# Kernel tuning notes

Measured on AMD Instinct MI355X. Metric: run time of the kernel, lower is better.

The kernel has to match this reference:

```python
import jax, jax.numpy as jnp
import numpy as np

T, K, V, B = 12, 50, 5000, 256
RHO, HT, HE = 300, 800, 256
DELTA, LAM = 0.005, 0.01
CLIP_LO, CLIP_HI = -100.0, 100.0


def setup_inputs():
    key = jax.random.key(0)
    ks = jax.random.split(key, 16)
    s = 0.02  # weight init scale
    rn = lambda k, sh, sc=s: jax.random.normal(k, sh) * sc
    return dict(
        normalized_bows=jax.random.uniform(ks[0], (B, V)),
        bow_t=jax.random.uniform(ks[1], (B, T, V)),
        adj_mat=jax.random.uniform(ks[2], (V, V)) * 0.01,
        mu_q_alpha=rn(ks[3], (K, T, RHO), 0.1),
        logsigma_q_alpha=rn(ks[4], (K, T, RHO), 0.1),
        rho_W=rn(ks[5], (V, RHO)), rho_b=jnp.zeros((V,)),
        qt_W1=rn(ks[6], (HT, V + K)), qt_b1=jnp.zeros((HT,)),
        qt_W2=rn(ks[7], (HT, HT)), qt_b2=jnp.zeros((HT,)),
        mut_W=rn(ks[8], (K, HT)), mut_b=jnp.zeros((K,)),
        lst_W=rn(ks[9], (K, HT)), lst_b=jnp.zeros((K,)),
        qe_W=rn(ks[10], (HE, V)), qe_b=jnp.zeros((HE,)),
        Wih=rn(ks[11], (4 * HE, HE)), Whh=rn(ks[12], (4 * HE, HE)),
        bih=jnp.zeros((4 * HE,)), bhh=jnp.zeros((4 * HE,)),
        mue_W=rn(ks[13], (K, HE + K)), mue_b=jnp.zeros((K,)),
        lse_W=rn(ks[14], (K, HE + K)), lse_b=jnp.zeros((K,)),
    )


def _kl(q_mu, q_ls, p_mu, p_ls):
    # KL(N(q_mu, e^{q_ls}) || N(p_mu, e^{p_ls})), logsigma == log-variance as in the torch code
    q_ls = jnp.clip(q_ls, CLIP_LO, CLIP_HI)
    kl = (jnp.exp(q_ls) + (q_mu - p_mu) ** 2) / (jnp.exp(p_ls) + 1e-6) - 1.0 + p_ls - q_ls
    return 0.5 * kl.sum(-1).mean()


def _forward(normalized_bows, bow_t, adj_mat, mu_q_alpha, logsigma_q_alpha,
             rho_W, rho_b, qt_W1, qt_b1, qt_W2, qt_b2, mut_W, mut_b,
             lst_W, lst_b, qe_W, qe_b, Wih, Whh, bih, bhh,
             mue_W, mue_b, lse_W, lse_b):
    ek = jax.random.split(jax.random.key(42), 3)

    # ---- get_alpha: samples are t-independent, KL chains through previous sample ----
    mu_a = jnp.transpose(mu_q_alpha, (1, 0, 2))        # [T,K,R]
    ls_a = jnp.transpose(logsigma_q_alpha, (1, 0, 2))  # [T,K,R]
    eps_a = jax.random.normal(ek[0], (T, K, RHO))
    alphas = mu_a + eps_a * jnp.exp(0.5 * ls_a)        # [T,K,R]
    p_mu_a = jnp.concatenate([jnp.zeros((1, K, RHO)), alphas[:-1]], 0)
    p_ls_a = jnp.concatenate([jnp.zeros((1, 1, 1)),
                              jnp.full((T - 1, 1, 1), jnp.log(DELTA))], 0)
    q_ls = jnp.clip(ls_a, CLIP_LO, CLIP_HI)
    kl_a = (jnp.exp(q_ls) + (mu_a - p_mu_a) ** 2) / (jnp.exp(p_ls_a) + 1e-6) - 1.0 + p_ls_a - q_ls
    kld_alpha = (0.5 * kl_a.sum(-1).mean(-1)).mean()   # per-t mean over K, then mean over T

    # ---- get_beta: rho Linear + softmax over vocab -> [T,K,V] ----
    beta = jax.nn.softmax(jnp.einsum('tkr,vr->tkv', alphas, rho_W) + rho_b, axis=-1)

    # ---- get_eta: LSTM over time + sequential reparameterized recurrence ----
    inp = jnp.einsum('btv,hv->bth', bow_t, qe_W) + qe_b  # [B,T,HE]

    def lstm_step(carry, x_t):
        h, c = carry
        g = x_t @ Wih.T + bih + h @ Whh.T + bhh          # [B,4HE]
        i, f, gg, o = jnp.split(g, 4, axis=-1)           # PyTorch gate order i,f,g,o
        c = jax.nn.sigmoid(f) * c + jax.nn.sigmoid(i) * jnp.tanh(gg)
        h = jax.nn.sigmoid(o) * jnp.tanh(c)
        return (h, c), h

    h0 = (jnp.zeros((B, HE)), jnp.zeros((B, HE)))
    _, lstm_out = jax.lax.scan(lstm_step, h0, jnp.transpose(inp, (1, 0, 2)))  # [T,B,HE]

    eps_e = jax.random.normal(ek[1], (T, B, K))
    # prior log-variance: 0 at t=0 (N(0,I)), log(delta) afterwards
    p_ls_e = jnp.concatenate([jnp.zeros((1,)), jnp.full((T - 1,), jnp.log(DELTA))])

    def eta_step(eta_prev, xs):
        o_t, eps_t, pls_t = xs
        z = jnp.concatenate([o_t, eta_prev], -1)         # [B,HE+K]
        mu = z @ mue_W.T + mue_b
        ls = z @ lse_W.T + lse_b
        eta_t = mu + eps_t * jnp.exp(0.5 * ls)
        kl_t = _kl(mu, ls, eta_prev, pls_t)              # eta_prev==0 at t=0, matching torch
        return eta_t, (eta_t, kl_t)

    _, (etas, kl_e) = jax.lax.scan(eta_step, jnp.zeros((B, K)), (lstm_out, eps_e, p_ls_e))
    kld_eta = kl_e.sum()                                  # etas: [T,B,K]

    # ---- get_theta: MLP encoder (enc_drop=0 -> dropout branch skipped) ----
    bows = jnp.broadcast_to(normalized_bows, (T, B, V))
    x = jnp.concatenate([bows, etas], -1)                 # [T,B,V+K]
    h = jax.nn.relu(x @ qt_W1.T + qt_b1)
    h = jax.nn.relu(h @ qt_W2.T + qt_b2)
    mu_t = h @ mut_W.T + mut_b
    ls_t = h @ lst_W.T + lst_b
    z = mu_t + jax.random.normal(ek[2], (T, B, K)) * jnp.exp(0.5 * ls_t)
    theta = jax.nn.softmax(z, axis=-1)                    # [T,B,K]
    kld_theta = _kl(mu_t, ls_t, etas, jnp.zeros((K,)))

    # ---- decode / nll ----
    bow_tT = jnp.transpose(bow_t, (1, 0, 2))              # [T,B,V]
    lik = jnp.einsum('tbk,tkv->tbv', theta, beta)
    nll = (10.0 * (-(jnp.log(lik + 1e-6)) * bow_tT).sum(-1).mean(-1)).sum()

    # ---- adjacency constraint: -lambda * trace(beta_t @ A @ beta_t^T) summed over t ----
    tmp = jnp.einsum('tkv,vw->tkw', beta, adj_mat)
    cond_loss = (-(LAM * (tmp * beta).sum((1, 2)))).sum()

    return nll, kld_theta, kld_alpha, kld_eta, cond_loss


def reference(normalized_bows, bow_t, adj_mat, mu_q_alpha, logsigma_q_alpha,
              rho_W, rho_b, qt_W1, qt_b1, qt_W2, qt_b2, mut_W, mut_b,
              lst_W, lst_b, qe_W, qe_b, Wih, Whh, bih, bhh,
              mue_W, mue_b, lse_W, lse_b):
    return _forward(normalized_bows, bow_t, adj_mat, mu_q_alpha, logsigma_q_alpha,
                    rho_W, rho_b, qt_W1, qt_b1, qt_W2, qt_b2, mut_W, mut_b,
                    lst_W, lst_b, qe_W, qe_b, Wih, Whh, bih, bhh,
                    mue_W, mue_b, lse_W, lse_b)
```

## Files before the change

### kernel.cpp

```cpp
#include <hip/hip_runtime.h>
#include <stdint.h>

#define TT 12
#define KK 50
#define VV 5000
#define BB 256
#define RHO_ 300
#define HT_ 800
#define HE_ 256
#define LOG_DELTA -5.2983174f
#define DENOM0 (1.0f + 1e-6f)
#define DENOM1 (0.005f + 1e-6f)

typedef __attribute__((ext_vector_type(8))) short short8;
typedef __attribute__((ext_vector_type(4))) float f32x4;

__host__ __device__ inline void threefry2x32(uint32_t k0, uint32_t k1,
                                             uint32_t x0, uint32_t x1,
                                             uint32_t& o0, uint32_t& o1) {
  uint32_t ks2 = k0 ^ k1 ^ 0x1BD11BDAu;
  x0 += k0; x1 += k1;
#define TF_RND(r) { x0 += x1; x1 = (x1 << r) | (x1 >> (32 - r)); x1 ^= x0; }
  TF_RND(13) TF_RND(15) TF_RND(26) TF_RND(6)  x0 += k1;  x1 += ks2 + 1u;
  TF_RND(17) TF_RND(29) TF_RND(16) TF_RND(24) x0 += ks2; x1 += k0 + 2u;
  TF_RND(13) TF_RND(15) TF_RND(26) TF_RND(6)  x0 += k0;  x1 += k1 + 3u;
  TF_RND(17) TF_RND(29) TF_RND(16) TF_RND(24) x0 += k1;  x1 += ks2 + 4u;
  TF_RND(13) TF_RND(15) TF_RND(26) TF_RND(6)  x0 += ks2; x1 += k0 + 5u;
#undef TF_RND
  o0 = x0; o1 = x1;
}

__device__ inline float erfinv_f(float x) {
  float w = -log1pf(-x * x);
  float p;
  if (w < 5.0f) {
    w -= 2.5f;
    p = 2.81022636e-08f;
    p = fmaf(p, w, 3.43273939e-07f);
    p = fmaf(p, w, -3.5233877e-06f);
    p = fmaf(p, w, -4.39150654e-06f);
    p = fmaf(p, w, 0.00021858087f);
    p = fmaf(p, w, -0.00125372503f);
    p = fmaf(p, w, -0.00417768164f);
    p = fmaf(p, w, 0.246640727f);
    p = fmaf(p, w, 1.50140941f);
  } else {
    w = sqrtf(w) - 3.0f;
    p = -0.000200214257f;
    p = fmaf(p, w, 0.000100950558f);
    p = fmaf(p, w, 0.00134934322f);
    p = fmaf(p, w, -0.00367342844f);
    p = fmaf(p, w, 0.00573950773f);
    p = fmaf(p, w, -0.0076224613f);
    p = fmaf(p, w, 0.00943887047f);
    p = fmaf(p, w, 1.00167406f);
    p = fmaf(p, w, 2.83297682f);
  }
  return p * x;
}

__device__ inline float jax_normal_f(uint32_t k0, uint32_t k1, uint32_t idx) {
  uint32_t o0, o1, bits;
  threefry2x32(k0, k1, 0u, idx, o0, o1);
  bits = o0 ^ o1;
  float f = __uint_as_float((bits >> 9) | 0x3f800000u) - 1.0f;
  const float lo = -0.99999994f;
  float u = fmaf(f, 2.0f, lo);
  u = fmaxf(lo, u);
  return 1.41421356f * erfinv_f(u);
}

__device__ inline float sigmoidf_(float x) { return 1.0f / (1.0f + expf(-x)); }

__device__ inline short f2bf(float f) {
  uint32_t x = __float_as_uint(f);
  uint32_t r = (x + 0x7fffu + ((x >> 16) & 1u)) >> 16;
  return (short)r;
}
__device__ inline float bf2f(short u) {
  return __uint_as_float(((uint32_t)(uint16_t)u) << 16);
}

__device__ inline void blockReduceAtomicAdd(float v, double* target, float* redbuf) {
  int lane = threadIdx.x & 63, wid = threadIdx.x >> 6;
  #pragma unroll
  for (int off = 32; off; off >>= 1) v += __shfl_down(v, off, 64);
  if (lane == 0) redbuf[wid] = v;
  __syncthreads();
  if (threadIdx.x == 0) {
    float tot = redbuf[0] + redbuf[1] + redbuf[2] + redbuf[3];
    atomicAdd(target, (double)tot);
  }
}

template<int MODE, int AF32>
__global__ __launch_bounds__(256) void mfma_gemm(
    const void* __restrict__ Ap, const short* __restrict__ Bp,
    float* __restrict__ C, const float* __restrict__ bias,
    const short* __restrict__ aux, double* __restrict__ slot,
    int M, int N, int K, int lda, int ldb, int ldc, int ldaux,
    int kchunk, int relu)
{
  __shared__ alignas(16) short As[128 * 40];
  __shared__ alignas(16) short Bs[128 * 40];
  __shared__ float redg[4];
  int tid = threadIdx.x, lane = tid & 63, wv = tid >> 6;
  int wm = wv >> 1, wn = wv & 1;
  int quad = lane >> 4, l16 = lane & 15;
  int m0 = blockIdx.y * 128, n0 = blockIdx.x * 128;
  int kbeg = (kchunk > 0) ? (int)blockIdx.z * kchunk : 0;
  int kend = (kchunk > 0) ? min(K, kbeg + kchunk) : K;
  const short* Ab = (const short*)Ap;
  const float* Af = (const float*)Ap;

  f32x4 acc[16];
  #pragma unroll
  for (int i = 0; i < 16; i++) acc[i] = (f32x4){0.f, 0.f, 0.f, 0.f};

  int srow = tid >> 2, skc = (tid & 3) * 8;
  for (int k0 = kbeg; k0 < kend; k0 += 32) {
    #pragma unroll
    for (int p = 0; p < 2; p++) {
      int row = srow + p * 64;
      int gk = k0 + skc;
      int rem = kend - gk;
      short8 av = {0, 0, 0, 0, 0, 0, 0, 0};
      int gm = m0 + row;
      if (gm < M && rem > 0) {
        if (AF32) {
          const float* s = Af + (size_t)gm * lda + gk;
          if (rem >= 8) {
            float4 f0 = *(const float4*)(s);
            float4 f1 = *(const float4*)(s + 4);
            av[0] = f2bf(f0.x); av[1] = f2bf(f0.y); av[2] = f2bf(f0.z); av[3] = f2bf(f0.w);
            av[4] = f2bf(f1.x); av[5] = f2bf(f1.y); av[6] = f2bf(f1.z); av[7] = f2bf(f1.w);
          } else {
            for (int e = 0; e < 8; e++) if (e < rem) av[e] = f2bf(s[e]);
          }
        } else {
          const short* s = Ab + (size_t)gm * lda + gk;
          if (rem >= 8) {
            const uint32_t* u = (const uint32_t*)s;
            uint32_t u0 = u[0], u1 = u[1], u2 = u[2], u3 = u[3];
            av[0] = (short)u0; av[1] = (short)(u0 >> 16);
            av[2] = (short)u1; av[3] = (short)(u1 >> 16);
            av[4] = (short)u2; av[5] = (short)(u2 >> 16);
            av[6] = (short)u3; av[7] = (short)(u3 >> 16);
          } else {
            for (int e = 0; e < 8; e++) if (e < rem) av[e] = s[e];
          }
        }
      }
      *(short8*)(&As[row * 40 + skc]) = av;
      short8 bv = {0, 0, 0, 0, 0, 0, 0, 0};
      int gn = n0 + row;
      if (gn < N && rem > 0) {
        const short* s = Bp + (size_t)gn * ldb + gk;
        if (rem >= 8) {
          const uint32_t* u = (const uint32_t*)s;
          uint32_t u0 = u[0], u1 = u[1], u2 = u[2], u3 = u[3];
          bv[0] = (short)u0; bv[1] = (short)(u0 >> 16);
          bv[2] = (short)u1; bv[3] = (short)(u1 >> 16);
          bv[4] = (short)u2; bv[5] = (short)(u2 >> 16);
          bv[6] = (short)u3; bv[7] = (short)(u3 >> 16);
        } else {
          for (int e = 0; e < 8; e++) if (e < rem) bv[e] = s[e];
        }
      }
      *(short8*)(&Bs[row * 40 + skc]) = bv;
    }
    __syncthreads();
    short8 af[4], bfr[4];
    const short* ap = &As[(wm * 64 + l16) * 40 + quad * 8];
    const short* bp = &Bs[(wn * 64 + l16) * 40 + quad * 8];
    #pragma unroll
    for (int i = 0; i < 4; i++) af[i] = *(const short8*)(ap + i * 16 * 40);
    #pragma unroll
    for (int j = 0; j < 4; j++) bfr[j] = *(const short8*)(bp + j * 16 * 40);
    #pragma unroll
    for (int i = 0; i < 4; i++)
      #pragma unroll
      for (int j = 0; j < 4; j++)
        acc[i * 4 + j] = __builtin_amdgcn_mfma_f32_16x16x32_bf16(af[i], bfr[j], acc[i * 4 + j], 0, 0, 0);
    __syncthreads();
  }

  float s = 0.f;
  #pragma unroll
  for (int i = 0; i < 4; i++) {
    int gmb = m0 + wm * 64 + i * 16 + quad * 4;
    #pragma unroll
    for (int j = 0; j < 4; j++) {
      int gn = n0 + wn * 64 + j * 16 + l16;
      f32x4 v = acc[i * 4 + j];
      if (gn >= N) continue;
      if (MODE == 0) {
        float bs = bias ? bias[gn] : 0.f;
        #pragma unroll
        for (int r = 0; r < 4; r++) {
          int gm = gmb + r;
          if (gm < M) {
            float c = v[r] + bs;
            if (relu) c = fmaxf(c, 0.f);
            C[(size_t)gm * ldc + gn] = c;
          }
        }
      } else if (MODE == 1) {
        #pragma unroll
        for (int r = 0; r < 4; r++) {
          int gm = gmb + r;
          if (gm < M) atomicAdd(&C[(size_t)gm * ldc + gn], v[r]);
        }
      } else {
        #pragma unroll
        for (int r = 0; r < 4; r++) {
          int gm = gmb + r;
          if (gm < M) s += v[r] * bf2f(aux[(size_t)gm * ldaux + gn]);
        }
      }
    }
  }
  if (MODE == 2) {
    #pragma unroll
    for (int off = 32; off; off >>= 1) s += __shfl_down(s, off, 64);
    if (lane == 0) redg[wv] = s;
    __syncthreads();
    if (tid == 0) atomicAdd(slot, (double)(redg[0] + redg[1] + redg[2] + redg[3]));
  }
}

__global__ __launch_bounds__(256) void k_decode64(
    const short* __restrict__ theta_bf, const short* __restrict__ betaT,
    const float* __restrict__ bow_t, double* __restrict__ slot) {
  __shared__ alignas(16) short As[64 * 40];
  __shared__ alignas(16) short Bs[64 * 40];
  __shared__ float redg[4];
  int tid = threadIdx.x, lane = tid & 63, wv = tid >> 6;
  int wm = wv >> 1, wn = wv & 1;
  int quad = lane >> 4, l16 = lane & 15;
  int n0 = blockIdx.x * 64, m0 = blockIdx.y * 64, z = blockIdx.z;
  const short* A = theta_bf + (size_t)z * 256 * 56;

  f32x4 acc[2][2];
  #pragma unroll
  for (int i = 0; i < 2; i++)
    #pragma unroll
    for (int j = 0; j < 2; j++) acc[i][j] = (f32x4){0.f, 0.f, 0.f, 0.f};

  int srow = tid >> 2, skc = (tid & 3) * 8;
  #pragma unroll
  for (int k0 = 0; k0 < 64; k0 += 32) {
    int gk = k0 + skc, rem = KK - gk;
    short8 av = {0, 0, 0, 0, 0, 0, 0, 0};
    int gm = m0 + srow;
    if (rem > 0) {
      const short* s = A + (size_t)gm * 56 + gk;
      if (rem >= 8) {
        const uint32_t* u = (const uint32_t*)s;
        uint32_t u0 = u[0], u1 = u[1], u2 = u[2], u3 = u[3];
        av[0] = (short)u0; av[1] = (short)(u0 >> 16);
        av[2] = (short)u1; av[3] = (short)(u1 >> 16);
        av[4] = (short)u2; av[5] = (short)(u2 >> 16);
        av[6] = (short)u3; av[7] = (short)(u3 >> 16);
      } else {
        for (int e = 0; e < 8; e++) if (e < rem) av[e] = s[e];
      }
    }
    *(short8*)(&As[srow * 40 + skc]) = av;
    short8 bv = {0, 0, 0, 0, 0, 0, 0, 0};
    int gn = n0 + srow;
    if (gn < VV && rem > 0) {
      const short* s = betaT + (size_t)gn * 600 + z * KK + gk;
      if (rem >= 8) {
        const uint32_t* u = (const uint32_t*)s;
        uint32_t u0 = u[0], u1 = u[1], u2 = u[2], u3 = u[3];
        bv[0] = (short)u0; bv[1] = (short)(u0 >> 16);
        bv[2] = (short)u1; bv[3] = (short)(u1 >> 16);
        bv[4] = (short)u2; bv[5] = (short)(u2 >> 16);
        bv[6] = (short)u3; bv[7] = (short)(u3 >> 16);
      } else {
        for (int e = 0; e < 8; e++) if (e < rem) bv[e] = s[e];
      }
    }
    *(short8*)(&Bs[srow * 40 + skc]) = bv;
    __syncthreads();
    short8 af[2], bfr[2];
    #pragma unroll
    for (int i = 0; i < 2; i++) af[i] = *(const short8*)(&As[(wm * 32 + i * 16 + l16) * 40 + quad * 8]);
    #pragma unroll
    for (int j = 0; j < 2; j++) bfr[j] = *(const short8*)(&Bs[(wn * 32 + j * 16 + l16) * 40 + quad * 8]);
    #pragma unroll
    for (int i = 0; i < 2; i++)
      #pragma unroll
      for (int j = 0; j < 2; j++)
        acc[i][j] = __builtin_amdgcn_mfma_f32_16x16x32_bf16(af[i], bfr[j], acc[i][j], 0, 0, 0);
    __syncthreads();
  }

  float s = 0.f;
  #pragma unroll
  for (int i = 0; i < 2; i++) {
    int gmb = m0 + wm * 32 + i * 16 + quad * 4;
    #pragma unroll
    for (int j = 0; j < 2; j++) {
      int gn = n0 + wn * 32 + j * 16 + l16;
      if (gn >= VV) continue;
      f32x4 v = acc[i][j];
      #pragma unroll
      for (int r = 0; r < 4; r++) {
        int gm = gmb + r;
        s -= __logf(v[r] + 1e-6f) * bow_t[((size_t)gm * TT + z) * VV + gn];
      }
    }
  }
  #pragma unroll
  for (int off = 32; off; off >>= 1) s += __shfl_down(s, off, 64);
  if (lane == 0) redg[wv] = s;
  __syncthreads();
  if (tid == 0) atomicAdd(slot, (double)(redg[0] + redg[1] + redg[2] + redg[3]));
}

__global__ void k_prep(const float* __restrict__ qe_W, const float* __restrict__ Wih,
                       const float* __restrict__ qt_W2, const float* __restrict__ qt_W1,
                       const float* __restrict__ rho_W, const float* __restrict__ Whh,
                       const float* __restrict__ bih, const float* __restrict__ bhh,
                       const float* __restrict__ qe_b, const float* __restrict__ qt_b1,
                       const float* __restrict__ mut_W, const float* __restrict__ mut_b,
                       const float* __restrict__ lst_W, const float* __restrict__ lst_b,
                       short* __restrict__ qeW_bf, short* __restrict__ Wih_bf,
                       short* __restrict__ qtW2_bf, short* __restrict__ qtW1_bf,
                       short* __restrict__ tail_bf, short* __restrict__ rhoW_bf,
                       float* __restrict__ whhT, float* __restrict__ sumbias,
                       float* __restrict__ inp, float* __restrict__ bows_part,
                       short* __restrict__ headW_bf, float* __restrict__ head_b) {
  const int N0 = 1280000, N1 = 262144, N2 = 640000, N3 = 4000000, N4 = 40000,
            N5 = 1500000, N6 = 262144, N7 = 1024, N8 = 786432, N9 = 204800,
            N10 = 80000, N11 = 100;
  const int total = N0 + N1 + N2 + N3 + N4 + N5 + N6 + N7 + N8 + N9 + N10 + N11;
  for (int i = blockIdx.x * 256 + threadIdx.x; i < total; i += gridDim.x * 256) {
    int idx = i;
    if (idx < N0) { qeW_bf[idx] = f2bf(qe_W[idx]); continue; }
    idx -= N0;
    if (idx < N1) { Wih_bf[idx] = f2bf(Wih[idx]); continue; }
    idx -= N1;
    if (idx < N2) { qtW2_bf[idx] = f2bf(qt_W2[idx]); continue; }
    idx -= N2;
    if (idx < N3) { int r = idx / VV, c = idx % VV;
      qtW1_bf[idx] = f2bf(qt_W1[(size_t)r * (VV + KK) + c]); continue; }
    idx -= N3;
    if (idx < N4) { int r = idx / KK, c = idx % KK;
      tail_bf[idx] = f2bf(qt_W1[(size_t)r * (VV + KK) + VV + c]); continue; }
    idx -= N4;
    if (idx < N5) { rhoW_bf[idx] = f2bf(rho_W[idx]); continue; }
    idx -= N5;
    if (idx < N6) { int h = idx >> 10, j = idx & 1023;
      whhT[idx] = Whh[(size_t)j * HE_ + h]; continue; }
    idx -= N6;
    if (idx < N7) { sumbias[idx] = bih[idx] + bhh[idx]; continue; }
    idx -= N7;
    if (idx < N8) { inp[idx] = qe_b[idx & 255]; continue; }
    idx -= N8;
    if (idx < N9) { bows_part[idx] = qt_b1[idx % 800]; continue; }
    idx -= N9;
    if (idx < N10) { int r = idx / HT_, c = idx % HT_;
      headW_bf[idx] = f2bf(r < KK ? mut_W[(size_t)r * HT_ + c]
                                  : lst_W[(size_t)(r - KK) * HT_ + c]); continue; }
    idx -= N10;
    head_b[idx] = (idx < KK) ? mut_b[idx] : lst_b[idx - KK];
  }
}

__global__ void k_alphas(const float* __restrict__ mu_q, const float* __restrict__ ls_q,
                         short* __restrict__ alph_bf, double* __restrict__ acc,
                         uint32_t ka, uint32_t kb) {
  __shared__ float red[4];
  int i = blockIdx.x * 256 + threadIdx.x;
  float kl = 0.f;
  if (i < TT * KK * RHO_) {
    int t = i / (KK * RHO_);
    int k = (i / RHO_) % KK;
    int r = i % RHO_;
    int src = k * (TT * RHO_) + t * RHO_ + r;
    float mu = mu_q[src], ls = ls_q[src];
    float eps = jax_normal_f(ka, kb, (uint32_t)i);
    float a = mu + eps * expf(0.5f * ls);
    alph_bf[i] = f2bf(a);
    float qls = fminf(fmaxf(ls, -100.f), 100.f);
    float pmu = 0.f, pls = 0.f, denom = DENOM0;
    if (t > 0) {
      int srcp = k * (TT * RHO_) + (t - 1) * RHO_ + r;
      float mup = mu_q[srcp], lsp = ls_q[srcp];
      float epsp = jax_normal_f(ka, kb, (uint32_t)(i - KK * RHO_));
      pmu = mup + epsp * expf(0.5f * lsp);
      pls = LOG_DELTA; denom = DENOM1;
    }
    float d = mu - pmu;
    kl = (expf(qls) + d * d) / denom - 1.0f + pls - qls;
  }
  blockReduceAtomicAdd(kl, &acc[2], red);
}

__global__ void k_softmax_bf(const float* __restrict__ in, short* __restrict__ out, int ncols) {
  int row = blockIdx.x;
  const float* d = in + (size_t)row * ncols;
  short* o = out + (size_t)row * ncols;
  int tid = threadIdx.x;
  __shared__ float red[256];
  float m = -INFINITY;
  for (int v = tid; v < ncols; v += 256) m = fmaxf(m, d[v]);
  red[tid] = m; __syncthreads();
  for (int s = 128; s; s >>= 1) { if (tid < s) red[tid] = fmaxf(red[tid], red[tid + s]); __syncthreads(); }
  float mx = red[0]; __syncthreads();
  float sum = 0.f;
  for (int v = tid; v < ncols; v += 256) sum += __expf(d[v] - mx);
  red[tid] = sum; __syncthreads();
  for (int s = 128; s; s >>= 1) { if (tid < s) red[tid] += red[tid + s]; __syncthreads(); }
  float inv = 1.0f / red[0];
  for (int v = tid; v < ncols; v += 256) o[v] = f2bf(__expf(d[v] - mx) * inv);
}

__global__ __launch_bounds__(256) void k_transpose_bf(const short* __restrict__ in,
                                                      short* __restrict__ out, int R, int Cc) {
  __shared__ short tile[32][33];
  int c0 = blockIdx.x * 32, r0 = blockIdx.y * 32;
  int tx = threadIdx.x & 31, ty = threadIdx.x >> 5;
  for (int rr = ty; rr < 32; rr += 8) {
    int r = r0 + rr, c = c0 + tx;
    tile[rr][tx] = (r < R && c < Cc) ? in[(size_t)r * Cc + c] : (short)0;
  }
  __syncthreads();
  for (int cc = ty; cc < 32; cc += 8) {
    int c = c0 + cc, r = r0 + tx;
    if (c < Cc && r < R) out[(size_t)c * R + r] = tile[tx][cc];
  }
}

__global__ __launch_bounds__(1024) void k_lstm_all(
    const float* __restrict__ xg, const float* __restrict__ whhT,
    float* __restrict__ lstm_out) {
  __shared__ float hprev[4][256];
  __shared__ float g_s[4][1024];
  int tid = threadIdx.x;
  int b0 = blockIdx.x * 4;
  float c[4] = {0.f, 0.f, 0.f, 0.f};
  if (tid < 256) {
    #pragma unroll
    for (int bb = 0; bb < 4; bb++) hprev[bb][tid] = 0.f;
  }
  __syncthreads();
  for (int t = 0; t < TT; t++) {
    float a0 = 0.f, a1 = 0.f, a2 = 0.f, a3 = 0.f;
    #pragma unroll 8
    for (int h = 0; h < 256; h++) {
      float w = whhT[(size_t)h * 1024 + tid];
      a0 = fmaf(w, hprev[0][h], a0);
      a1 = fmaf(w, hprev[1][h], a1);
      a2 = fmaf(w, hprev[2][h], a2);
      a3 = fmaf(w, hprev[3][h], a3);
    }
    __syncthreads();
    g_s[0][tid] = xg[((size_t)(b0 + 0) * TT + t) * 1024 + tid] + a0;
    g_s[1][tid] = xg[((size_t)(b0 + 1) * TT + t) * 1024 + tid] + a1;
    g_s[2][tid] = xg[((size_t)(b0 + 2) * TT + t) * 1024 + tid] + a2;
    g_s[3][tid] = xg[((size_t)(b0 + 3) * TT + t) * 1024 + tid] + a3;
    __syncthreads();
    if (tid < 256) {
      #pragma unroll
      for (int bb = 0; bb < 4; bb++) {
        float gi = g_s[bb][tid], gf = g_s[bb][256 + tid];
        float gc = g_s[bb][512 + tid], go = g_s[bb][768 + tid];
        c[bb] = sigmoidf_(gf) * c[bb] + sigmoidf_(gi) * tanhf(gc);
        float h = sigmoidf_(go) * tanhf(c[bb]);
        hprev[bb][tid] = h;
        lstm_out[((size_t)t * BB + b0 + bb) * 256 + tid] = h;
      }
    }
    __syncthreads();
  }
}

__global__ __launch_bounds__(128) void k_eta_all(
    const float* __restrict__ lstm_out, const float* __restrict__ mue_W,
    const float* __restrict__ mue_b, const float* __restrict__ lse_W,
    const float* __restrict__ lse_b, float* __restrict__ etas,
    double* __restrict__ acc, uint32_t ka, uint32_t kb) {
  __shared__ float wmu[KK * 306];
  __shared__ float wls[KK * 306];
  __shared__ float z[HE_ + KK];
  __shared__ float mu_s[KK], ls_s[KK];
  int b = blockIdx.x, tid = threadIdx.x;
  for (int i = tid; i < KK * 306; i += 128) { wmu[i] = mue_W[i]; wls[i] = lse_W[i]; }
  float klsum = 0.f;
  if (tid < KK) z[HE_ + tid] = 0.f;
  __syncthreads();
  for (int t = 0; t < TT; t++) {
    for (int i = tid; i < HE_; i += 128) z[i] = lstm_out[((size_t)t * BB + b) * HE_ + i];
    __syncthreads();
    if (tid < 100) {
      int j = tid % KK; bool isMu = tid < KK;
      const float* w = (isMu ? wmu : wls) + j * 306;
      float a = 0.f, a2 = 0.f;
      for (int i = 0; i < HE_ + KK; i += 2) {
        a = fmaf(z[i], w[i], a);
        a2 = fmaf(z[i + 1], w[i + 1], a2);
      }
      a += a2 + (isMu ? mue_b : lse_b)[j];
      if (isMu) mu_s[j] = a; else ls_s[j] = a;
    }
    __syncthreads();
    if (tid < KK) {
      float mu = mu_s[tid], ls = ls_s[tid];
      float eps = jax_normal_f(ka, kb, (uint32_t)((t * BB + b) * KK + tid));
      float eta = mu + eps * expf(0.5f * ls);
      float qls = fminf(fmaxf(ls, -100.f), 100.f);
      float pmu = z[HE_ + tid];
      float pls = (t == 0) ? 0.f : LOG_DELTA;
      float denom = (t == 0) ? DENOM0 : DENOM1;
      float d = mu - pmu;
      klsum += (expf(qls) + d * d) / denom - 1.0f + pls - qls;
      etas[((size_t)t * BB + b) * KK + tid] = eta;
      z[HE_ + tid] = eta;
    }
    __syncthreads();
  }
  if (tid < 64) {
    #pragma unroll
    for (int off = 32; off; off >>= 1) klsum += __shfl_down(klsum, off, 64);
    if (tid == 0) atomicAdd(&acc[3], (double)klsum);
  }
}

__global__ __launch_bounds__(256) void k_h1(
    const float* __restrict__ etas, const short* __restrict__ tail_bf,
    const float* __restrict__ bows_part, short* __restrict__ h1_bf) {
  __shared__ float el[8][KK];
  int m0 = blockIdx.x * 8, tid = threadIdx.x;
  for (int idx = tid; idx < 8 * KK; idx += 256) {
    int mm = idx / KK, kk = idx % KK;
    el[mm][kk] = etas[(size_t)(m0 + mm) * KK + kk];
  }
  __syncthreads();
  for (int j = tid; j < HT_; j += 256) {
    const uint32_t* w = (const uint32_t*)(tail_bf + (size_t)j * KK);
    float wv[KK];
    #pragma unroll
    for (int k = 0; k < KK / 2; k++) {
      uint32_t u = w[k];
      wv[2 * k] = bf2f((short)u); wv[2 * k + 1] = bf2f((short)(u >> 16));
    }
    #pragma unroll
    for (int mm = 0; mm < 8; mm++) {
      int m = m0 + mm, b = m & (BB - 1);
      float a = bows_part[(size_t)b * HT_ + j];
      #pragma unroll
      for (int k = 0; k < KK; k++) a = fmaf(el[mm][k], wv[k], a);
      h1_bf[(size_t)m * HT_ + j] = f2bf(fmaxf(a, 0.f));
    }
  }
}

__global__ __launch_bounds__(64) void k_theta2(
    const float* __restrict__ mu_ls, const float* __restrict__ etas,
    short* __restrict__ theta_bf, double* __restrict__ acc, uint32_t ka, uint32_t kb) {
  int m = blockIdx.x, tid = threadIdx.x;
  float kl = 0.f, zv = -INFINITY;
  if (tid < KK) {
    float mu = mu_ls[(size_t)m * 100 + tid];
    float ls = mu_ls[(size_t)m * 100 + KK + tid];
    float eps = jax_normal_f(ka, kb, (uint32_t)(m * KK + tid));
    zv = mu + eps * expf(0.5f * ls);
    float qls = fminf(fmaxf(ls, -100.f), 100.f);
    float e = etas[(size_t)m * KK + tid];
    float d = mu - e;
    kl = (expf(qls) + d * d) / DENOM0 - 1.0f - qls;
  }
  float mx = zv;
  #pragma unroll
  for (int off = 32; off; off >>= 1) mx = fmaxf(mx, __shfl_xor(mx, off, 64));
  float ev = (tid < KK) ? expf(zv - mx) : 0.f;
  float sum = ev;
  #pragma unroll
  for (int off = 32; off; off >>= 1) sum += __shfl_xor(sum, off, 64);
  if (tid < KK) theta_bf[(size_t)m * 56 + tid] = f2bf(ev / sum);
  #pragma unroll
  for (int off = 32; off; off >>= 1) kl += __shfl_down(kl, off, 64);
  if (tid == 0) atomicAdd(&acc[1], (double)kl);
}

__global__ void k_final(const double* __restrict__ acc, float* __restrict__ out) {
  if (threadIdx.x == 0 && blockIdx.x == 0) {
    out[0] = (float)(acc[0] * (10.0 / (double)BB));
    out[1] = (float)(acc[1] * (0.5 / ((double)TT * (double)BB)));
    out[2] = (float)(acc[2] * (0.5 / ((double)TT * (double)KK)));
    out[3] = (float)(acc[3] * (0.5 / (double)BB));
    out[4] = (float)(acc[4] * (-0.01));
  }
}

extern "C" void kernel_launch(void* const* d_in, const int* in_sizes, int n_in,
                              void* d_out, int out_size, void* d_ws, size_t ws_size,
                              hipStream_t stream) {
  const float* normalized_bows = (const float*)d_in[0];
  const float* bow_t  = (const float*)d_in[1];
  const float* adj    = (const float*)d_in[2];
  const float* mu_q   = (const float*)d_in[3];
  const float* ls_q   = (const float*)d_in[4];
  const float* rho_W  = (const float*)d_in[5];
  const float* rho_b  = (const float*)d_in[6];
  const float* qt_W1  = (const float*)d_in[7];
  const float* qt_b1  = (const float*)d_in[8];
  const float* qt_W2  = (const float*)d_in[9];
  const float* qt_b2  = (const float*)d_in[10];
  const float* mut_W  = (const float*)d_in[11];
  const float* mut_b  = (const float*)d_in[12];
  const float* lst_W  = (const float*)d_in[13];
  const float* lst_b  = (const float*)d_in[14];
  const float* qe_W   = (const float*)d_in[15];
  const float* qe_b   = (const float*)d_in[16];
  const float* Wih    = (const float*)d_in[17];
  const float* Whh    = (const float*)d_in[18];
  const float* bih    = (const float*)d_in[19];
  const float* bhh    = (const float*)d_in[20];
  const float* mue_W  = (const float*)d_in[21];
  const float* mue_b  = (const float*)d_in[22];
  const float* lse_W  = (const float*)d_in[23];
  const float* lse_b  = (const float*)d_in[24];
  float* out = (float*)d_out;

  double* acc = (double*)d_ws;
  float* p          = (float*)d_ws + 16;
  float* betaT_f    = p;               p += 1500000;
  float* beta_bf_f  = p;               p += 1500000;
  float* alphbf_f   = p;               p += 90000;
  float* rhoWbf_f   = p;               p += 750000;
  float* arenaA     = p;               p += 3145728;
  float* qeWbf_f    = p;               p += 640000;
  float* Wihbf_f    = p;               p += 131072;
  float* arenaB     = p;               p += 2320000;
  float* tailbf_f   = p;               p += 20000;
  float* poolC      = p;               p += 2621440;
  float* sumbias    = p;               p += 1024;
  float* etas       = p;               p += 153600;
  float* bows_part  = p;               p += 204800;
  float* thbf_f     = p;               p += 86016;
  float* headWbf_f  = p;               p += 40000;
  float* head_b     = p;               p += 104;
  float* mu_ls      = p;               p += 307200;

  short* betaT    = (short*)betaT_f;
  short* beta_bf  = (short*)beta_bf_f;
  short* alph_bf  = (short*)alphbf_f;
  short* rhoW_bf  = (short*)rhoWbf_f;
  float* logits   = arenaA;
  float* xg       = arenaA;
  short* qeW_bf   = (short*)qeWbf_f;
  short* Wih_bf   = (short*)Wihbf_f;
  short* qtW1_bf  = (short*)arenaB;
  short* qtW2_bf  = (short*)(arenaB + 2000000);
  short* h1_bf    = (short*)arenaB;
  short* tail_bf  = (short*)tailbf_f;
  float* inp      = poolC;
  float* whhT     = poolC + 786432;
  float* lstm_out = poolC + 786432 + 1048576;
  float* h2       = poolC;
  short* theta_bf = (short*)thbf_f;
  short* headW_bf = (short*)headWbf_f;

  uint32_t e0a, e0b, e1a, e1b, e2a, e2b;
  threefry2x32(0u, 42u, 0u, 0u, e0a, e0b);
  threefry2x32(0u, 42u, 0u, 1u, e1a, e1b);
  threefry2x32(0u, 42u, 0u, 2u, e2a, e2b);

  (void)hipMemsetAsync(acc, 0, 5 * sizeof(double), stream);

  k_prep<<<8192, 256, 0, stream>>>(qe_W, Wih, qt_W2, qt_W1, rho_W, Whh, bih, bhh,
                                   qe_b, qt_b1, mut_W, mut_b, lst_W, lst_b,
                                   qeW_bf, Wih_bf, qtW2_bf, qtW1_bf, tail_bf, rhoW_bf,
                                   whhT, sumbias, inp, bows_part, headW_bf, head_b);

  k_alphas<<<704, 256, 0, stream>>>(mu_q, ls_q, alph_bf, acc, e0a, e0b);

  mfma_gemm<0, 0><<<dim3(40, 5), 256, 0, stream>>>(alph_bf, rhoW_bf, logits, rho_b,
      nullptr, nullptr, 600, VV, RHO_, RHO_, RHO_, VV, 0, 0, 0);
  k_softmax_bf<<<600, 256, 0, stream>>>(logits, beta_bf, VV);
  k_transpose_bf<<<dim3(157, 19), 256, 0, stream>>>(beta_bf, betaT, 600, VV);

  mfma_gemm<2, 1><<<dim3(5, 40, 8), 256, 0, stream>>>(adj, beta_bf, nullptr, nullptr,
      betaT, acc + 4, VV, 600, VV, VV, VV, 0, 600, 640, 0);

  mfma_gemm<1, 1><<<dim3(2, 24, 8), 256, 0, stream>>>(bow_t, qeW_bf, inp, nullptr,
      nullptr, nullptr, 3072, HE_, VV, VV, VV, HE_, 0, 640, 0);
  mfma_gemm<0, 1><<<dim3(8, 24), 256, 0, stream>>>(inp, Wih_bf, xg, sumbias,
      nullptr, nullptr, 3072, 1024, HE_, HE_, HE_, 1024, 0, 0, 0);

  k_lstm_all<<<64, 1024, 0, stream>>>(xg, whhT, lstm_out);
  k_eta_all<<<BB, 128, 0, stream>>>(lstm_out, mue_W, mue_b, lse_W, lse_b, etas, acc, e1a, e1b);

  mfma_gemm<1, 1><<<dim3(7, 2, 8), 256, 0, stream>>>(normalized_bows, qtW1_bf, bows_part,
      nullptr, nullptr, nullptr, BB, HT_, VV, VV, VV, HT_, 0, 640, 0);
  k_h1<<<384, 256, 0, stream>>>(etas, tail_bf, bows_part, h1_bf);
  mfma_gemm<0, 0><<<dim3(7, 24), 256, 0, stream>>>(h1_bf, qtW2_bf, h2, qt_b2,
      nullptr, nullptr, 3072, HT_, HT_, HT_, HT_, HT_, 0, 0, 1);
  mfma_gemm<0, 1><<<dim3(1, 24), 256, 0, stream>>>(h2, headW_bf, mu_ls, head_b,
      nullptr, nullptr, 3072, 100, HT_, HT_, HT_, 100, 0, 0, 0);
  k_theta2<<<3072, 64, 0, stream>>>(mu_ls, etas, theta_bf, acc, e2a, e2b);

  k_decode64<<<dim3(79, 4, 12), 256, 0, stream>>>(theta_bf, betaT, bow_t, acc);

  k_final<<<1, 64, 0, stream>>>(acc, out);
}
```

Baseline: 1.065 ms.

## Add dedicated cond-loss kernel reading each adj tile once across all beta columns

The adjacency trace term moves out of the generic 128x128 GEMM into a dedicated kernel. Each block takes a 64-row strip of adj and accumulates against all 600 beta rows (5 N-tiles) in registers, so the 100MB fp32 adj matrix is read and converted to bf16 once instead of five times. The split-K factor for the bow_t and normalized_bows GEMMs also doubles (kchunk 640 to 320, z 8 to 16) to raise parallelism, at the cost of more atomic adds. The new kernel uses large LDS (about 56KB) and 160 accumulator registers per thread, which may lower occupancy.

```diff
diff --git a/kernel.cpp b/kernel.cpp
--- a/kernel.cpp
+++ b/kernel.cpp
@@ -97,13 +97,11 @@
 __global__ __launch_bounds__(256) void mfma_gemm(
     const void* __restrict__ Ap, const short* __restrict__ Bp,
     float* __restrict__ C, const float* __restrict__ bias,
-    const short* __restrict__ aux, double* __restrict__ slot,
-    int M, int N, int K, int lda, int ldb, int ldc, int ldaux,
+    int M, int N, int K, int lda, int ldb, int ldc,
     int kchunk, int relu)
 {
   __shared__ alignas(16) short As[128 * 40];
   __shared__ alignas(16) short Bs[128 * 40];
-  __shared__ float redg[4];
   int tid = threadIdx.x, lane = tid & 63, wv = tid >> 6;
   int wm = wv >> 1, wn = wv & 1;
   int quad = lane >> 4, l16 = lane & 15;
@@ -185,7 +183,6 @@
     __syncthreads();
   }
 
-  float s = 0.f;
   #pragma unroll
   for (int i = 0; i < 4; i++) {
     int gmb = m0 + wm * 64 + i * 16 + quad * 4;
@@ -205,28 +202,120 @@
             C[(size_t)gm * ldc + gn] = c;
           }
         }
-      } else if (MODE == 1) {
+      } else {
         #pragma unroll
         for (int r = 0; r < 4; r++) {
           int gm = gmb + r;
           if (gm < M) atomicAdd(&C[(size_t)gm * ldc + gn], v[r]);
         }
+      }
+    }
+  }
+}
+
+__global__ __launch_bounds__(256) void k_cond2(
+    const float* __restrict__ adj, const short* __restrict__ beta_bf,
+    const short* __restrict__ betaT, double* __restrict__ slot, int kchunk) {
+  __shared__ alignas(16) short As[64 * 40];
+  __shared__ alignas(16) short Bs[5][128 * 40];
+  __shared__ float redg[4];
+  int tid = threadIdx.x, lane = tid & 63, wv = tid >> 6;
+  int wm = wv & 1, wn = wv >> 1;
+  int quad = lane >> 4, l16 = lane & 15;
+  int m0 = blockIdx.x * 64;
+  int z = blockIdx.y;
+  int kbeg = z * kchunk, kend = min(VV, kbeg + kchunk);
+
+  f32x4 acc[5][8];
+  #pragma unroll
+  for (int nt = 0; nt < 5; nt++)
+    #pragma unroll
+    for (int i = 0; i < 8; i++) acc[nt][i] = (f32x4){0.f, 0.f, 0.f, 0.f};
+
+  int srow = tid >> 2, skc = (tid & 3) * 8;
+  for (int k0 = kbeg; k0 < kend; k0 += 32) {
+    int gk = k0 + skc, rem = kend - gk;
+    short8 av = {0, 0, 0, 0, 0, 0, 0, 0};
+    int gm = m0 + srow;
+    if (gm < VV && rem > 0) {
+      const float* s = adj + (size_t)gm * VV + gk;
+      if (rem >= 8) {
+        float4 f0 = *(const float4*)(s);
+        float4 f1 = *(const float4*)(s + 4);
+        av[0] = f2bf(f0.x); av[1] = f2bf(f0.y); av[2] = f2bf(f0.z); av[3] = f2bf(f0.w);
+        av[4] = f2bf(f1.x); av[5] = f2bf(f1.y); av[6] = f2bf(f1.z); av[7] = f2bf(f1.w);
       } else {
+        for (int e = 0; e < 8; e++) if (e < rem) av[e] = f2bf(s[e]);
+      }
+    }
+    *(short8*)(&As[srow * 40 + skc]) = av;
+    #pragma unroll
+    for (int nt = 0; nt < 5; nt++) {
+      #pragma unroll
+      for (int p = 0; p < 2; p++) {
+        int row = srow + p * 64;
+        int gn = nt * 128 + row;
+        short8 bv = {0, 0, 0, 0, 0, 0, 0, 0};
+        if (gn < 600 && rem > 0) {
+          const short* s = beta_bf + (size_t)gn * VV + gk;
+          if (rem >= 8) {
+            const uint32_t* u = (const uint32_t*)s;
+            uint32_t u0 = u[0], u1 = u[1], u2 = u[2], u3 = u[3];
+            bv[0] = (short)u0; bv[1] = (short)(u0 >> 16);
+            bv[2] = (short)u1; bv[3] = (short)(u1 >> 16);
+            bv[4] = (short)u2; bv[5] = (short)(u2 >> 16);
+            bv[6] = (short)u3; bv[7] = (short)(u3 >> 16);
+          } else {
+            for (int e = 0; e < 8; e++) if (e < rem) bv[e] = s[e];
+          }
+        }
+        *(short8*)(&Bs[nt][row * 40 + skc]) = bv;
+      }
+    }
+    __syncthreads();
+    short8 af[2];
+    const short* ap = &As[(wm * 32 + l16) * 40 + quad * 8];
+    af[0] = *(const short8*)(ap);
+    af[1] = *(const short8*)(ap + 16 * 40);
+    #pragma unroll
+    for (int nt = 0; nt < 5; nt++) {
+      short8 bfr[4];
+      const short* bp = &Bs[nt][(wn * 64 + l16) * 40 + quad * 8];
+      #pragma unroll
+      for (int j = 0; j < 4; j++) bfr[j] = *(const short8*)(bp + j * 16 * 40);
+      #pragma unroll
+      for (int i = 0; i < 2; i++)
+        #pragma unroll
+        for (int j = 0; j < 4; j++)
+          acc[nt][i * 4 + j] = __builtin_amdgcn_mfma_f32_16x16x32_bf16(af[i], bfr[j], acc[nt][i * 4 + j], 0, 0, 0);
+    }
+    __syncthreads();
+  }
+
+  float s = 0.f;
+  #pragma unroll
+  for (int nt = 0; nt < 5; nt++) {
+    #pragma unroll
+    for (int i = 0; i < 2; i++) {
+      int gmb = m0 + wm * 32 + i * 16 + quad * 4;
+      #pragma unroll
+      for (int j = 0; j < 4; j++) {
+        int gn = nt * 128 + wn * 64 + j * 16 + l16;
+        if (gn >= 600) continue;
+        f32x4 v = acc[nt][i * 4 + j];
         #pragma unroll
         for (int r = 0; r < 4; r++) {
           int gm = gmb + r;
-          if (gm < M) s += v[r] * bf2f(aux[(size_t)gm * ldaux + gn]);
+          if (gm < VV) s += v[r] * bf2f(betaT[(size_t)gm * 600 + gn]);
         }
       }
     }
   }
-  if (MODE == 2) {
-    #pragma unroll
-    for (int off = 32; off; off >>= 1) s += __shfl_down(s, off, 64);
-    if (lane == 0) redg[wv] = s;
-    __syncthreads();
-    if (tid == 0) atomicAdd(slot, (double)(redg[0] + redg[1] + redg[2] + redg[3]));
-  }
+  #pragma unroll
+  for (int off = 32; off; off >>= 1) s += __shfl_down(s, off, 64);
+  if (lane == 0) redg[wv] = s;
+  __syncthreads();
+  if (tid == 0) atomicAdd(slot, (double)(redg[0] + redg[1] + redg[2] + redg[3]));
 }
 
 __global__ __launch_bounds__(256) void k_decode64(
@@ -681,28 +770,27 @@
   k_alphas<<<704, 256, 0, stream>>>(mu_q, ls_q, alph_bf, acc, e0a, e0b);
 
   mfma_gemm<0, 0><<<dim3(40, 5), 256, 0, stream>>>(alph_bf, rhoW_bf, logits, rho_b,
-      nullptr, nullptr, 600, VV, RHO_, RHO_, RHO_, VV, 0, 0, 0);
+      600, VV, RHO_, RHO_, RHO_, VV, 0, 0);
   k_softmax_bf<<<600, 256, 0, stream>>>(logits, beta_bf, VV);
   k_transpose_bf<<<dim3(157, 19), 256, 0, stream>>>(beta_bf, betaT, 600, VV);
 
-  mfma_gemm<2, 1><<<dim3(5, 40, 8), 256, 0, stream>>>(adj, beta_bf, nullptr, nullptr,
-      betaT, acc + 4, VV, 600, VV, VV, VV, 0, 600, 640, 0);
-
-  mfma_gemm<1, 1><<<dim3(2, 24, 8), 256, 0, stream>>>(bow_t, qeW_bf, inp, nullptr,
-      nullptr, nullptr, 3072, HE_, VV, VV, VV, HE_, 0, 640, 0);
+  k_cond2<<<dim3(79, 8), 256, 0, stream>>>(adj, beta_bf, betaT, acc + 4, 625);
+
+  mfma_gemm<1, 1><<<dim3(2, 24, 16), 256, 0, stream>>>(bow_t, qeW_bf, inp, nullptr,
+      3072, HE_, VV, VV, VV, HE_, 320, 0);
   mfma_gemm<0, 1><<<dim3(8, 24), 256, 0, stream>>>(inp, Wih_bf, xg, sumbias,
-      nullptr, nullptr, 3072, 1024, HE_, HE_, HE_, 1024, 0, 0, 0);
+      3072, 1024, HE_, HE_, HE_, 1024, 0, 0);
 
   k_lstm_all<<<64, 1024, 0, stream>>>(xg, whhT, lstm_out);
   k_eta_all<<<BB, 128, 0, stream>>>(lstm_out, mue_W, mue_b, lse_W, lse_b, etas, acc, e1a, e1b);
 
-  mfma_gemm<1, 1><<<dim3(7, 2, 8), 256, 0, stream>>>(normalized_bows, qtW1_bf, bows_part,
-      nullptr, nullptr, nullptr, BB, HT_, VV, VV, VV, HT_, 0, 640, 0);
+  mfma_gemm<1, 1><<<dim3(7, 2, 16), 256, 0, stream>>>(normalized_bows, qtW1_bf, bows_part,
+      nullptr, BB, HT_, VV, VV, VV, HT_, 320, 0);
   k_h1<<<384, 256, 0, stream>>>(etas, tail_bf, bows_part, h1_bf);
   mfma_gemm<0, 0><<<dim3(7, 24), 256, 0, stream>>>(h1_bf, qtW2_bf, h2, qt_b2,
-      nullptr, nullptr, 3072, HT_, HT_, HT_, HT_, HT_, 0, 0, 1);
+      3072, HT_, HT_, HT_, HT_, HT_, 0, 1);
   mfma_gemm<0, 1><<<dim3(1, 24), 256, 0, stream>>>(h2, headW_bf, mu_ls, head_b,
-      nullptr, nullptr, 3072, 100, HT_, HT_, HT_, 100, 0, 0, 0);
+      3072, 100, HT_, HT_, HT_, 100, 0, 0);
   k_theta2<<<3072, 64, 0, stream>>>(mu_ls, etas, theta_bf, acc, e2a, e2b);
 
   k_decode64<<<dim3(79, 4, 12), 256, 0, stream>>>(theta_bf, betaT, bow_t, acc);
```

Result: slower. 1.270 ms (+19.3%).
